# Kernel optimization log

Hardware: AMD Instinct MI355X
Metric: run time of the kernel (lower is better)

The kernel has to match this reference:

```python
import jax, jax.numpy as jnp
import numpy as np
import math

B, T, D = 2, 2048, 2048
H, KV, HD = 16, 4, 128  # n_heads, n_kv_heads, head_dim
ROPE_BASE = 10000.0


def setup_inputs() -> dict:
    key = jax.random.key(0)
    ks = jax.random.split(key, 5)
    s = 0.02
    return {
        "x": jax.random.normal(ks[0], (B, T, D), dtype=jnp.float32),
        "Wq": jax.random.normal(ks[1], (D, H * HD), dtype=jnp.float32) * s,
        "Wk": jax.random.normal(ks[2], (D, KV * HD), dtype=jnp.float32) * s,
        "Wv": jax.random.normal(ks[3], (D, KV * HD), dtype=jnp.float32) * s,
        "Wo": jax.random.normal(ks[4], (H * HD, D), dtype=jnp.float32) * s,
    }


def _rope_tables(t_len, dtype):
    inv_freq = 1.0 / (ROPE_BASE ** (jnp.arange(0, HD, 2, dtype=jnp.float32) / HD))
    t = jnp.arange(t_len, dtype=jnp.float32)
    freqs = t[:, None] * inv_freq[None, :]  # [T, HD/2]
    return jnp.cos(freqs).astype(dtype), jnp.sin(freqs).astype(dtype)


def _apply_rope(x, cos, sin):
    # x: [B, h, T, HD]; cos/sin: [T, HD/2] broadcast to [1,1,T,HD/2]
    c = cos[None, None, :, :]
    s = sin[None, None, :, :]
    x1, x2 = x[..., ::2], x[..., 1::2]
    rot = jnp.stack([x1 * c - x2 * s, x1 * s + x2 * c], axis=-1)  # interleave back
    return rot.reshape(x.shape)


def reference(x, Wq, Wk, Wv, Wo):
    b, t, d = x.shape
    q = (x @ Wq).reshape(b, t, H, HD).transpose(0, 2, 1, 3)   # [B,H,T,HD]
    k = (x @ Wk).reshape(b, t, KV, HD).transpose(0, 2, 1, 3)  # [B,KV,T,HD]
    v = (x @ Wv).reshape(b, t, KV, HD).transpose(0, 2, 1, 3)

    cos, sin = _rope_tables(t, x.dtype)
    q = _apply_rope(q, cos, sin)
    k = _apply_rope(k, cos, sin)

    rep = H // KV
    k_rep = jnp.repeat(k, rep, axis=1)  # [B,H,T,HD]
    v_rep = jnp.repeat(v, rep, axis=1)

    scale = 1.0 / math.sqrt(HD)
    scores = jnp.einsum("bhqd,bhkd->bhqk", q, k_rep) * scale
    causal = jnp.triu(jnp.ones((t, t), dtype=bool), k=1)
    neg = jnp.finfo(scores.dtype).min
    scores = jnp.where(causal[None, None, :, :], neg, scores)
    attn = jax.nn.softmax(scores, axis=-1)
    out = jnp.einsum("bhqk,bhkd->bhqd", attn, v_rep)
    y = out.transpose(0, 2, 1, 3).reshape(b, t, H * HD) @ Wo
    return y
```

## Files before the change

kernel.cpp:

```cpp
#include <hip/hip_runtime.h>
#include <cstdint>
#include <math.h>

#define T_SEQ 2048
#define BATCH 2
#define NH 16
#define NKV 4
#define HD 128

typedef __attribute__((ext_vector_type(8))) short short8;
typedef __attribute__((ext_vector_type(4))) float f32x4;

__device__ __forceinline__ ushort f2bf(float f) {
  uint32_t u = __builtin_bit_cast(uint32_t, f);
  u += 0x7FFF + ((u >> 16) & 1);
  return (ushort)(u >> 16);
}
__device__ __forceinline__ ushort f2bf_trunc(float f) {
  return (ushort)(__builtin_bit_cast(uint32_t, f) >> 16);
}
__device__ __forceinline__ float bf2f(ushort u) {
  uint32_t v = ((uint32_t)u) << 16;
  return __builtin_bit_cast(float, v);
}
__device__ __forceinline__ void ld16(void* lds, const void* g) {
  __builtin_amdgcn_global_load_lds((const __attribute__((address_space(1))) void*)g,
                                   (__attribute__((address_space(3))) void*)lds,
                                   16, 0, 0);
}

__global__ __launch_bounds__(256) void prep(
    const float* __restrict__ x, ushort* __restrict__ xb,
    const float* __restrict__ Wq, const float* __restrict__ Wk,
    const float* __restrict__ Wv, const float* __restrict__ Wo,
    ushort* __restrict__ wqkvT, ushort* __restrict__ woT) {
  __shared__ float tile[32][33];
  const int bid = blockIdx.x;
  const int tid = threadIdx.x;
  if (bid < 8192) {
    int i = (bid * 256 + tid) * 4;
    float4 v = *(const float4*)&x[i];
    ushort4 o;
    o.x = f2bf(v.x); o.y = f2bf(v.y); o.z = f2bf(v.z); o.w = f2bf(v.w);
    *(ushort4*)&xb[i] = o;
    return;
  }
  const float* in;
  ushort* out;
  int N, lid;
  if (bid < 12288)      { in = Wq; out = wqkvT;                        N = 2048; lid = bid - 8192; }
  else if (bid < 13312) { in = Wk; out = wqkvT + (size_t)2048 * 2048;  N = 512;  lid = bid - 12288; }
  else if (bid < 14336) { in = Wv; out = wqkvT + (size_t)2560 * 2048;  N = 512;  lid = bid - 13312; }
  else                  { in = Wo; out = woT;                          N = 2048; lid = bid - 14336; }
  const int K = 2048;
  const int nb = N / 32;
  const int n0 = (lid % nb) * 32, k0 = (lid / nb) * 32;
  const int r = tid >> 3, c4 = (tid & 7) << 2;
  float4 v = *(const float4*)&in[(size_t)(k0 + r) * N + n0 + c4];
  tile[r][c4 + 0] = v.x; tile[r][c4 + 1] = v.y;
  tile[r][c4 + 2] = v.z; tile[r][c4 + 3] = v.w;
  __syncthreads();
  ushort4 o;
  o.x = f2bf(tile[c4 + 0][r]); o.y = f2bf(tile[c4 + 1][r]);
  o.z = f2bf(tile[c4 + 2][r]); o.w = f2bf(tile[c4 + 3][r]);
  *(ushort4*)&out[(size_t)(n0 + r) * K + k0 + c4] = o;
}

template <typename OutT>
__global__ __launch_bounds__(256) void gemm_bt(const ushort* __restrict__ A,
                                               const ushort* __restrict__ Bt,
                                               OutT* __restrict__ C,
                                               int M, int N, int K) {
  __shared__ __align__(16) ushort As[128 * 32];
  __shared__ __align__(16) ushort Bs[128 * 32];
  const int tid = threadIdx.x;
  const int w = tid >> 6, l = tid & 63;
  const int wr = w >> 1, wc = w & 1;
  const int quad = l >> 4, l15 = l & 15;
  const int bm = blockIdx.y * 128, bn = blockIdx.x * 128;

  f32x4 acc[4][4];
#pragma unroll
  for (int mi = 0; mi < 4; ++mi)
#pragma unroll
    for (int ni = 0; ni < 4; ++ni)
#pragma unroll
      for (int r = 0; r < 4; ++r) acc[mi][ni][r] = 0.f;

  for (int k0 = 0; k0 < K; k0 += 32) {
    __syncthreads();
#pragma unroll
    for (int j = 0; j < 2; ++j) {
      int r0 = w * 32 + j * 16;
      int row = r0 + (l >> 2);
      int gc = (l & 3) ^ ((row >> 1) & 3);
      ld16(&As[r0 * 32], &A[(size_t)(bm + row) * K + k0 + gc * 8]);
      ld16(&Bs[r0 * 32], &Bt[(size_t)(bn + row) * K + k0 + gc * 8]);
    }
    __syncthreads();
    short8 af[4], bf[4];
#pragma unroll
    for (int mi = 0; mi < 4; ++mi) {
      int m = wr * 64 + mi * 16 + l15;
      af[mi] = *(const short8*)&As[m * 32 + (quad ^ ((m >> 1) & 3)) * 8];
    }
#pragma unroll
    for (int ni = 0; ni < 4; ++ni) {
      int n = wc * 64 + ni * 16 + l15;
      bf[ni] = *(const short8*)&Bs[n * 32 + (quad ^ ((n >> 1) & 3)) * 8];
    }
#pragma unroll
    for (int mi = 0; mi < 4; ++mi)
#pragma unroll
      for (int ni = 0; ni < 4; ++ni)
        acc[mi][ni] = __builtin_amdgcn_mfma_f32_16x16x32_bf16(af[mi], bf[ni], acc[mi][ni], 0, 0, 0);
  }
#pragma unroll
  for (int mi = 0; mi < 4; ++mi)
#pragma unroll
    for (int ni = 0; ni < 4; ++ni)
#pragma unroll
      for (int r = 0; r < 4; ++r) {
        int grow = bm + wr * 64 + mi * 16 + quad * 4 + r;
        int gcol = bn + wc * 64 + ni * 16 + l15;
        if constexpr (__is_same(OutT, ushort))
          C[(size_t)grow * N + gcol] = f2bf(acc[mi][ni][r]);
        else
          C[(size_t)grow * N + gcol] = acc[mi][ni][r];
      }
}

__global__ __launch_bounds__(256) void rope_k_bf16(ushort* __restrict__ qkv) {
  int idx = blockIdx.x * 256 + threadIdx.x;
  const int PAIRS_PER_ROW = 256;
  if (idx >= BATCH * T_SEQ * PAIRS_PER_ROW) return;
  int row = idx >> 8;
  int kp = idx & 255;
  int t = row & (T_SEQ - 1);
  int i = kp & 63;
  ushort* ptr = qkv + (size_t)row * 3072 + 2048 + 2 * kp;
  float inv = expf((float)i * -0.14391156831212788f);
  float ang = (float)t * inv;
  float sn, cs;
  sincosf(ang, &sn, &cs);
  float x1 = bf2f(ptr[0]), x2 = bf2f(ptr[1]);
  ptr[0] = f2bf(x1 * cs - x2 * sn);
  ptr[1] = f2bf(x1 * sn + x2 * cs);
}

__global__ __launch_bounds__(256) void transpose_v(const ushort* __restrict__ qkv,
                                                   ushort* __restrict__ vT) {
  __shared__ ushort tile[32][34];
  int m0 = blockIdx.x * 32, d0 = blockIdx.y * 32;
  int r = threadIdx.x >> 3, c4 = (threadIdx.x & 7) << 2;
  ushort4 v = *(const ushort4*)&qkv[(size_t)(m0 + r) * 3072 + 2560 + d0 + c4];
  tile[r][c4 + 0] = v.x; tile[r][c4 + 1] = v.y;
  tile[r][c4 + 2] = v.z; tile[r][c4 + 3] = v.w;
  __syncthreads();
  ushort4 o;
  o.x = tile[c4 + 0][r]; o.y = tile[c4 + 1][r];
  o.z = tile[c4 + 2][r]; o.w = tile[c4 + 3][r];
  *(ushort4*)&vT[(size_t)(d0 + r) * 4096 + m0 + c4] = o;
}

__global__ __launch_bounds__(512, 2) void attn_mfma(const ushort* __restrict__ qkv,
                                                    const ushort* __restrict__ vT,
                                                    ushort* __restrict__ ao) {
  __shared__ __align__(16) ushort Ks[2][64 * 128];
  __shared__ __align__(16) ushort Vt[2][128 * 64];
  __shared__ __align__(16) ushort Ps[8][16 * 64];
  const int tid = threadIdx.x;
  const int w = tid >> 6, l = tid & 63;
  const int quad = l >> 4, l15 = l & 15;
  const int hw = w >> 1, sub = w & 1;
  const int kvh = blockIdx.y, b = blockIdx.z;
  const int h = kvh * 4 + hw;
  const size_t krow0 = (size_t)b * T_SEQ;
  const float SC = 0.12751744595764253f;

  ushort* pw = Ps[w];
  const int within = l & 7;
  const int colbase = l15 >> 3;

  auto stage = [&](int kt, int bufi) {
    const int kt0 = kt << 6;
    ushort* kb = Ks[bufi];
    ushort* vb = Vt[bufi];
#pragma unroll
    for (int j = 0; j < 2; ++j) {
      int r0 = w * 8 + j * 4;
      int row = r0 + (l >> 4);
      int gc = (l & 15) ^ ((row >> 1) & 7);
      ld16(&kb[r0 * 128], &qkv[(krow0 + kt0 + row) * 3072 + 2048 + kvh * 128 + gc * 8]);
    }
#pragma unroll
    for (int j = 0; j < 2; ++j) {
      int r0 = w * 16 + j * 8;
      int row = r0 + (l >> 3);
      int gc = (l & 7) ^ (row & 7);
      ld16(&vb[r0 * 64], &vT[(size_t)(kvh * 128 + row) * 4096 + krow0 + kt0 + gc * 8]);
    }
  };

  const int bx = blockIdx.x;
  int qt = (bx & 1) ? (63 - (bx >> 1)) : (bx >> 1);
  if (b == 1) qt = 63 - qt;
  const int qt0 = qt << 5;
  const size_t qrow0 = krow0 + qt0;

  const int t_pos = qt0 + sub * 16 + l15;
  short8 qf[4];
#pragma unroll
  for (int kc = 0; kc < 4; ++kc) {
    short8 raw = *(const short8*)&qkv[(qrow0 + sub * 16 + l15) * 3072 + h * 128 + kc * 32 + quad * 8];
#pragma unroll
    for (int u = 0; u < 4; ++u) {
      int i_idx = kc * 16 + quad * 4 + u;
      float inv = expf((float)i_idx * -0.14391156831212788f);
      float sn, cs;
      sincosf((float)t_pos * inv, &sn, &cs);
      cs *= SC; sn *= SC;
      float x1 = bf2f((ushort)raw[2 * u]);
      float x2 = bf2f((ushort)raw[2 * u + 1]);
      qf[kc][2 * u]     = (short)f2bf(x1 * cs - x2 * sn);
      qf[kc][2 * u + 1] = (short)f2bf(x1 * sn + x2 * cs);
    }
  }

  f32x4 oacc[8];
#pragma unroll
  for (int i = 0; i < 8; ++i)
#pragma unroll
    for (int r = 0; r < 4; ++r) oacc[i][r] = 0.f;
  float lpart[4] = {0.f, 0.f, 0.f, 0.f};

  const int nkt = (qt >> 1) + 1;
  stage(0, 0);
  for (int kt = 0; kt < nkt; ++kt) {
    __syncthreads();
    if (kt + 1 < nkt) stage(kt + 1, (kt + 1) & 1);
    const ushort* kb = Ks[kt & 1];
    const ushort* vb = Vt[kt & 1];

    f32x4 sacc[4];
#pragma unroll
    for (int ni = 0; ni < 4; ++ni)
#pragma unroll
      for (int r = 0; r < 4; ++r) sacc[ni][r] = 0.f;
#pragma unroll
    for (int kc = 0; kc < 4; ++kc) {
#pragma unroll
      for (int ni = 0; ni < 4; ++ni) {
        int n = ni * 16 + l15;
        short8 bfr = *(const short8*)&kb[n * 128 + ((kc * 4 + quad) ^ ((n >> 1) & 7)) * 8];
        sacc[ni] = __builtin_amdgcn_mfma_f32_16x16x32_bf16(qf[kc], bfr, sacc[ni], 0, 0, 0);
      }
    }

    const int kt0 = kt << 6;
    if (kt == nkt - 1) {
      const int rowg = qt0 + sub * 16 + quad * 4;
#pragma unroll
      for (int ni = 0; ni < 4; ++ni) {
        const int colid = kt0 + ni * 16 + l15;
#pragma unroll
        for (int r = 0; r < 4; ++r) {
          float s = (colid > rowg + r) ? -1e30f : sacc[ni][r];
          float pv = __builtin_amdgcn_exp2f(s);
          lpart[r] += pv;
          int prow = quad * 4 + r;
          pw[prow * 64 + (((ni * 2 + colbase) ^ (prow & 7)) << 3) + within] = f2bf_trunc(pv);
        }
      }
    } else {
#pragma unroll
      for (int ni = 0; ni < 4; ++ni)
#pragma unroll
        for (int r = 0; r < 4; ++r) {
          float pv = __builtin_amdgcn_exp2f(sacc[ni][r]);
          lpart[r] += pv;
          int prow = quad * 4 + r;
          pw[prow * 64 + (((ni * 2 + colbase) ^ (prow & 7)) << 3) + within] = f2bf_trunc(pv);
        }
    }

#pragma unroll
    for (int kc = 0; kc < 2; ++kc) {
      short8 a = *(const short8*)&pw[l15 * 64 + ((kc * 4 + quad) ^ (l15 & 7)) * 8];
#pragma unroll
      for (int ni2 = 0; ni2 < 8; ++ni2) {
        int d = ni2 * 16 + l15;
        short8 bfr = *(const short8*)&vb[d * 64 + ((kc * 4 + quad) ^ (d & 7)) * 8];
        oacc[ni2] = __builtin_amdgcn_mfma_f32_16x16x32_bf16(a, bfr, oacc[ni2], 0, 0, 0);
      }
    }
  }

#pragma unroll
  for (int r = 0; r < 4; ++r) {
    float lv = lpart[r];
    lv += __shfl_xor(lv, 1);
    lv += __shfl_xor(lv, 2);
    lv += __shfl_xor(lv, 4);
    lv += __shfl_xor(lv, 8);
    float inv = 1.f / lv;
    size_t grow = qrow0 + sub * 16 + quad * 4 + r;
#pragma unroll
    for (int ni2 = 0; ni2 < 8; ++ni2)
      ao[grow * 2048 + h * 128 + ni2 * 16 + l15] = f2bf(oacc[ni2][r] * inv);
  }
}

extern "C" void kernel_launch(void* const* d_in, const int* in_sizes, int n_in,
                              void* d_out, int out_size, void* d_ws, size_t ws_size,
                              hipStream_t stream) {
  const float* x  = (const float*)d_in[0];
  const float* Wq = (const float*)d_in[1];
  const float* Wk = (const float*)d_in[2];
  const float* Wv = (const float*)d_in[3];
  const float* Wo = (const float*)d_in[4];
  float* y = (float*)d_out;

  const int M = BATCH * T_SEQ;
  ushort* xb    = (ushort*)d_ws;
  ushort* wqkvT = xb + (size_t)M * 2048;
  ushort* woT   = wqkvT + (size_t)3072 * 2048;
  ushort* qkv   = woT + (size_t)2048 * 2048;
  ushort* vTb   = qkv + (size_t)M * 3072;
  ushort* aob   = vTb + (size_t)512 * 4096;

  prep<<<18432, 256, 0, stream>>>(x, xb, Wq, Wk, Wv, Wo, wqkvT, woT);

  gemm_bt<ushort><<<dim3(3072 / 128, M / 128), 256, 0, stream>>>(
      xb, wqkvT, qkv, M, 3072, 2048);

  rope_k_bf16<<<(M * 256 + 255) / 256, 256, 0, stream>>>(qkv);
  transpose_v<<<dim3(M / 32, 512 / 32), 256, 0, stream>>>(qkv, vTb);

  attn_mfma<<<dim3(64, NKV, BATCH), 512, 0, stream>>>(qkv, vTb, aob);

  gemm_bt<float><<<dim3(2048 / 128, M / 128), 256, 0, stream>>>(
      aob, woT, y, M, 2048, 2048);
}
```

Baseline: 329.8 us.

## Split attention blocks into head pairs, single-buffer K/V, add MFMA priority hints

Each attention block now handles 2 query heads instead of 4, with 256 threads, so the grid doubles to 64x8x2 blocks. K/V staging drops from double to single buffering, with a sync before and after each load. This cuts shared memory per block so more blocks can be resident, at the cost of K/V tiles being re-read per head pair and less load/compute overlap inside a block. It also adds s_setprio around the MFMA sections and changes the query-tile ordering to balance causal work across blocks.

New measurement: 405.1 us. 1.23x slower.

```diff
diff --git a/kernel.cpp b/kernel.cpp
--- a/kernel.cpp
+++ b/kernel.cpp
@@ -163,18 +163,18 @@
   *(ushort4*)&vT[(size_t)(d0 + r) * 4096 + m0 + c4] = o;
 }
 
-__global__ __launch_bounds__(512, 2) void attn_mfma(const ushort* __restrict__ qkv,
+__global__ __launch_bounds__(256, 4) void attn_mfma(const ushort* __restrict__ qkv,
                                                     const ushort* __restrict__ vT,
                                                     ushort* __restrict__ ao) {
-  __shared__ __align__(16) ushort Ks[2][64 * 128];
-  __shared__ __align__(16) ushort Vt[2][128 * 64];
-  __shared__ __align__(16) ushort Ps[8][16 * 64];
+  __shared__ __align__(16) ushort Ks[64 * 128];
+  __shared__ __align__(16) ushort Vt[128 * 64];
+  __shared__ __align__(16) ushort Ps[4][16 * 64];
   const int tid = threadIdx.x;
   const int w = tid >> 6, l = tid & 63;
   const int quad = l >> 4, l15 = l & 15;
   const int hw = w >> 1, sub = w & 1;
-  const int kvh = blockIdx.y, b = blockIdx.z;
-  const int h = kvh * 4 + hw;
+  const int kvh = blockIdx.y >> 1, hp = blockIdx.y & 1, b = blockIdx.z;
+  const int h = kvh * 4 + hp * 2 + hw;
   const size_t krow0 = (size_t)b * T_SEQ;
   const float SC = 0.12751744595764253f;
 
@@ -182,29 +182,28 @@
   const int within = l & 7;
   const int colbase = l15 >> 3;
 
-  auto stage = [&](int kt, int bufi) {
+  auto stage = [&](int kt) {
     const int kt0 = kt << 6;
-    ushort* kb = Ks[bufi];
-    ushort* vb = Vt[bufi];
-#pragma unroll
-    for (int j = 0; j < 2; ++j) {
-      int r0 = w * 8 + j * 4;
+#pragma unroll
+    for (int j = 0; j < 4; ++j) {
+      int r0 = w * 16 + j * 4;
       int row = r0 + (l >> 4);
       int gc = (l & 15) ^ ((row >> 1) & 7);
-      ld16(&kb[r0 * 128], &qkv[(krow0 + kt0 + row) * 3072 + 2048 + kvh * 128 + gc * 8]);
-    }
-#pragma unroll
-    for (int j = 0; j < 2; ++j) {
-      int r0 = w * 16 + j * 8;
+      ld16(&Ks[r0 * 128], &qkv[(krow0 + kt0 + row) * 3072 + 2048 + kvh * 128 + gc * 8]);
+    }
+#pragma unroll
+    for (int j = 0; j < 4; ++j) {
+      int r0 = w * 32 + j * 8;
       int row = r0 + (l >> 3);
       int gc = (l & 7) ^ (row & 7);
-      ld16(&vb[r0 * 64], &vT[(size_t)(kvh * 128 + row) * 4096 + krow0 + kt0 + gc * 8]);
+      ld16(&Vt[r0 * 64], &vT[(size_t)(kvh * 128 + row) * 4096 + krow0 + kt0 + gc * 8]);
     }
   };
 
   const int bx = blockIdx.x;
-  int qt = (bx & 1) ? (63 - (bx >> 1)) : (bx >> 1);
-  if (b == 1) qt = 63 - qt;
+  const int base = (bx & 1) | (((bx >> 2) & 1) << 1) | ((bx >> 3) << 2);
+  const int side = ((bx >> 1) ^ (bx >> 3)) & 1;
+  const int qt = side ? (63 - base) : base;
   const int qt0 = qt << 5;
   const size_t qrow0 = krow0 + qt0;
 
@@ -235,18 +234,19 @@
   float lpart[4] = {0.f, 0.f, 0.f, 0.f};
 
   const int nkt = (qt >> 1) + 1;
-  stage(0, 0);
   for (int kt = 0; kt < nkt; ++kt) {
+    if (kt) __syncthreads();
+    stage(kt);
     __syncthreads();
-    if (kt + 1 < nkt) stage(kt + 1, (kt + 1) & 1);
-    const ushort* kb = Ks[kt & 1];
-    const ushort* vb = Vt[kt & 1];
+    const ushort* kb = Ks;
+    const ushort* vb = Vt;
 
     f32x4 sacc[4];
 #pragma unroll
     for (int ni = 0; ni < 4; ++ni)
 #pragma unroll
       for (int r = 0; r < 4; ++r) sacc[ni][r] = 0.f;
+    __builtin_amdgcn_s_setprio(1);
 #pragma unroll
     for (int kc = 0; kc < 4; ++kc) {
 #pragma unroll
@@ -256,6 +256,7 @@
         sacc[ni] = __builtin_amdgcn_mfma_f32_16x16x32_bf16(qf[kc], bfr, sacc[ni], 0, 0, 0);
       }
     }
+    __builtin_amdgcn_s_setprio(0);
 
     const int kt0 = kt << 6;
     if (kt == nkt - 1) {
@@ -284,6 +285,7 @@
         }
     }
 
+    __builtin_amdgcn_s_setprio(1);
 #pragma unroll
     for (int kc = 0; kc < 2; ++kc) {
       short8 a = *(const short8*)&pw[l15 * 64 + ((kc * 4 + quad) ^ (l15 & 7)) * 8];
@@ -294,6 +296,7 @@
         oacc[ni2] = __builtin_amdgcn_mfma_f32_16x16x32_bf16(a, bfr, oacc[ni2], 0, 0, 0);
       }
     }
+    __builtin_amdgcn_s_setprio(0);
   }
 
 #pragma unroll
@@ -337,7 +340,7 @@
   rope_k_bf16<<<(M * 256 + 255) / 256, 256, 0, stream>>>(qkv);
   transpose_v<<<dim3(M / 32, 512 / 32), 256, 0, stream>>>(qkv, vTb);
 
-  attn_mfma<<<dim3(64, NKV, BATCH), 512, 0, stream>>>(qkv, vTb, aob);
+  attn_mfma<<<dim3(64, 8, BATCH), 256, 0, stream>>>(qkv, vTb, aob);
 
   gemm_bt<float><<<dim3(2048 / 128, M / 128), 256, 0, stream>>>(
       aob, woT, y, M, 2048, 2048);
```
